# Performance work log

Measured on AMD Instinct MI355X. Metric: run time of the kernel, lower is better.

Reference implementation:

```python
import jax, jax.numpy as jnp
import numpy as np

B, H, W, C = 16, 64, 64, 256
C8 = C // 8

def setup_inputs() -> dict:
    key = jax.random.key(0)
    ks = jax.random.split(key, 8)
    return {
        "x": jax.random.normal(ks[0], (B, H, W, C), dtype=jnp.float32),
        "Wf": jax.random.normal(ks[1], (C, C8), dtype=jnp.float32) * 0.05,
        "Wg": jax.random.normal(ks[2], (C, C8), dtype=jnp.float32) * 0.05,
        "Wh": jax.random.normal(ks[3], (C, C), dtype=jnp.float32) * 0.05,
        "bf": jax.random.normal(ks[4], (C8,), dtype=jnp.float32) * 0.05,
        "bg": jax.random.normal(ks[5], (C8,), dtype=jnp.float32) * 0.05,
        "bh": jax.random.normal(ks[6], (C,), dtype=jnp.float32) * 0.05,
        "gamma": jax.random.normal(ks[7], (1,), dtype=jnp.float32) * 0.05,
    }

def reference(x, Wf, Wg, Wh, bf, bg, bh, gamma):
    # 1x1 convs == per-pixel channel matmuls (NHWC)
    f = jnp.einsum('bhwc,cd->bhwd', x, Wf) + bf  # [B,H,W,C/8]
    g = jnp.einsum('bhwc,cd->bhwd', x, Wg) + bg  # [B,H,W,C/8]
    h = jnp.einsum('bhwc,cd->bhwd', x, Wh) + bh  # [B,H,W,C]
    b = x.shape[0]
    # K.batch_flatten flattens all non-batch dims -> attention over BATCH dim
    gf = g.reshape(b, -1)                      # [B, HWC/8]
    ff = f.reshape(b, -1)                      # [B, HWC/8]
    hf = h.reshape(b, -1)                      # [B, HWC]
    s = gf @ ff.T                              # [B, B]
    beta = jax.nn.softmax(s, axis=-1)          # softmax over batch axis
    o = (beta @ hf).reshape(x.shape)           # [B,H,W,C]
    # activation=None -> linear; gamma-scaled residual
    return gamma * o + x
```

## Files before the change

### kernel.cpp

```cpp
#include <hip/hip_runtime.h>

typedef __attribute__((ext_vector_type(4))) float  f4;
typedef __attribute__((ext_vector_type(2))) float  f2;
typedef __attribute__((ext_vector_type(8))) short  short8;
typedef __attribute__((ext_vector_type(4))) float  f32x4;
typedef __attribute__((ext_vector_type(2))) unsigned int u32x2;

static __device__ __forceinline__ unsigned short f2bf(float f) {
    unsigned u = __builtin_bit_cast(unsigned, f);
    unsigned r = (u + 0x7FFFu + ((u >> 16) & 1u)) >> 16;
    return (unsigned short)r;
}
static __device__ __forceinline__ float bf2f(unsigned short h) {
    return __builtin_bit_cast(float, ((unsigned)h) << 16);
}

__global__ __launch_bounds__(256) void k_setup(const float* __restrict__ Wh,
                                               const float* __restrict__ bh,
                                               const float* __restrict__ Wf,
                                               const float* __restrict__ Wg,
                                               const float* __restrict__ gamma,
                                               unsigned short* __restrict__ WhT,
                                               float* __restrict__ gb,
                                               unsigned short* __restrict__ Wfg_hi,
                                               unsigned short* __restrict__ Wfg_lo) {
    __shared__ float T[8 * 260];
    const int t = threadIdx.x, b = blockIdx.x;
    const float g = gamma[0];
    if (b < 32) {
        const int c0 = b * 8;
        const int cr = t >> 5, q = t & 31;
        f4 v0 = *(const f4*)(Wh + (c0 + cr) * 256 + q * 8);
        f4 v1 = *(const f4*)(Wh + (c0 + cr) * 256 + q * 8 + 4);
        *(f4*)(T + cr * 260 + q * 8)     = v0;
        *(f4*)(T + cr * 260 + q * 8 + 4) = v1;
        __syncthreads();
        short8 o;
        #pragma unroll
        for (int j = 0; j < 8; ++j) o[j] = (short)f2bf(g * T[j * 260 + t]);
        *(short8*)(WhT + t * 256 + c0) = o;
    } else {
        gb[t] = g * bh[t];
        const int n = t >> 2, cq = t & 3;
        const float* Wsrc = (n < 32) ? Wf : Wg;
        const int nn = n & 31;
        #pragma unroll
        for (int c8 = 0; c8 < 8; ++c8) {
            short8 h8, l8;
            #pragma unroll
            for (int k = 0; k < 8; ++k) {
                const int c = cq * 64 + c8 * 8 + k;
                const float v = Wsrc[c * 32 + nn];
                const unsigned short h = f2bf(v);
                h8[k] = (short)h;
                l8[k] = (short)f2bf(v - bf2f(h));
            }
            *(short8*)(Wfg_hi + n * 256 + cq * 64 + c8 * 8) = h8;
            *(short8*)(Wfg_lo + n * 256 + cq * 64 + c8 * 8) = l8;
        }
    }
}

__global__ __launch_bounds__(256, 2) void ka(const float* __restrict__ x,
                                             const unsigned short* __restrict__ Wfg_hi,
                                             const unsigned short* __restrict__ Wfg_lo,
                                             const unsigned short* __restrict__ WhT,
                                             const float* __restrict__ bfv,
                                             const float* __restrict__ bgv,
                                             float* __restrict__ s_part,
                                             unsigned short* __restrict__ Hb) {
    __shared__ __align__(16) unsigned char smem[65536];

    const int t = threadIdx.x, w = t >> 6, l = t & 63;
    const int p = blockIdx.x * 4 + w;

    f4 xr[16];
    #pragma unroll
    for (int j = 0; j < 16; ++j)
        xr[j] = *(const f4*)(x + (((j << 12) + p) << 8) + l * 4);
    #pragma unroll
    for (int j = 0; j < 16; ++j) {
        const int r = j * 4 + w;
        int bo = r * 512 + l * 8;
        bo ^= (r & 7) << 4;
        const unsigned short h0 = f2bf(xr[j][0]), h1 = f2bf(xr[j][1]);
        const unsigned short h2 = f2bf(xr[j][2]), h3 = f2bf(xr[j][3]);
        u32x2 ph, pl;
        ph[0] = ((unsigned)h1 << 16) | h0;
        ph[1] = ((unsigned)h3 << 16) | h2;
        const unsigned short e0 = f2bf(xr[j][0] - bf2f(h0));
        const unsigned short e1 = f2bf(xr[j][1] - bf2f(h1));
        const unsigned short e2 = f2bf(xr[j][2] - bf2f(h2));
        const unsigned short e3 = f2bf(xr[j][3] - bf2f(h3));
        pl[0] = ((unsigned)e1 << 16) | e0;
        pl[1] = ((unsigned)e3 << 16) | e2;
        *(u32x2*)(smem + bo)         = ph;
        *(u32x2*)(smem + 32768 + bo) = pl;
    }
    __syncthreads();

    const int lrow = l & 15;
    const int hi4 = l >> 4;
    const int kfe  = hi4 * 8;
    const int ncol = w * 16 + lrow;
    f32x4 acc[4];
    f32x4 hacc[4][4];
    #pragma unroll
    for (int mt = 0; mt < 4; ++mt) {
        acc[mt] = (f32x4){0.f, 0.f, 0.f, 0.f};
        #pragma unroll
        for (int nt = 0; nt < 4; ++nt) hacc[mt][nt] = (f32x4){0.f, 0.f, 0.f, 0.f};
    }

    #pragma unroll
    for (int k0 = 0; k0 < 256; k0 += 32) {
        const short8 bh_ = *(const short8*)(Wfg_hi + ncol * 256 + k0 + kfe);
        const short8 bl_ = *(const short8*)(Wfg_lo + ncol * 256 + k0 + kfe);
        short8 ah[4], al[4];
        #pragma unroll
        for (int mt = 0; mt < 4; ++mt) {
            const int row = mt * 16 + lrow;
            int bo = row * 512 + (k0 + kfe) * 2;
            bo ^= (row & 7) << 4;
            ah[mt] = *(const short8*)(smem + bo);
            al[mt] = *(const short8*)(smem + 32768 + bo);
        }
        #pragma unroll
        for (int mt = 0; mt < 4; ++mt) {
            acc[mt] = __builtin_amdgcn_mfma_f32_16x16x32_bf16(ah[mt], bh_, acc[mt], 0, 0, 0);
            acc[mt] = __builtin_amdgcn_mfma_f32_16x16x32_bf16(al[mt], bh_, acc[mt], 0, 0, 0);
            acc[mt] = __builtin_amdgcn_mfma_f32_16x16x32_bf16(ah[mt], bl_, acc[mt], 0, 0, 0);
        }
        if (Hb) {
            short8 hb_[4];
            #pragma unroll
            for (int nt = 0; nt < 4; ++nt)
                hb_[nt] = *(const short8*)(WhT + (w * 64 + nt * 16 + lrow) * 256 + k0 + kfe);
            #pragma unroll
            for (int mt = 0; mt < 4; ++mt)
                #pragma unroll
                for (int nt = 0; nt < 4; ++nt)
                    hacc[mt][nt] = __builtin_amdgcn_mfma_f32_16x16x32_bf16(
                        ah[mt], hb_[nt], hacc[mt][nt], 0, 0, 0);
        }
    }

    if (Hb) {
        __syncthreads();
        #pragma unroll
        for (int mt = 0; mt < 4; ++mt) {
            const int j = mt * 4 + hi4;
            #pragma unroll
            for (int nt = 0; nt < 4; ++nt) {
                const int d = w * 64 + nt * 16 + lrow;
                #pragma unroll
                for (int jj = 0; jj < 4; ++jj)
                    *(unsigned short*)(smem + (jj * 16 + j) * 544 + d * 2) =
                        f2bf(hacc[mt][nt][jj]);
            }
        }
        __syncthreads();
        {
            const int r = t >> 2, q = t & 3;
            const int px = r >> 4, j = r & 15;
            unsigned short* dst = Hb + ((size_t)j * 4096 + blockIdx.x * 4 + px) * 256;
            #pragma unroll
            for (int cc = 0; cc < 8; ++cc) {
                const int chunk = (q * 8 + cc + r) & 31;
                f4 v = *(const f4*)(smem + r * 544 + chunk * 16);
                *(f4*)(dst + chunk * 8) = v;
            }
        }
    }
    __syncthreads();

    float* FG = (float*)smem;
    const float bias = (ncol < 32) ? bfv[ncol] : bgv[ncol - 32];
    #pragma unroll
    for (int mt = 0; mt < 4; ++mt)
        #pragma unroll
        for (int jj = 0; jj < 4; ++jj) {
            const int row = mt * 16 + hi4 * 4 + jj;
            FG[row * 68 + ncol] = acc[mt][jj] + bias;
        }
    __syncthreads();

    const int si = t >> 4, sj = t & 15;
    float sacc = 0.f;
    #pragma unroll
    for (int q = 0; q < 4; ++q) {
        const float* Gp = FG + (si * 4 + q) * 68 + 32;
        const float* Fp = FG + (sj * 4 + q) * 68;
        #pragma unroll
        for (int d4 = 0; d4 < 8; ++d4) {
            f4 gv = *(const f4*)(Gp + d4 * 4);
            f4 fv = *(const f4*)(Fp + d4 * 4);
            sacc += gv[0] * fv[0] + gv[1] * fv[1] + gv[2] * fv[2] + gv[3] * fv[3];
        }
    }
    s_part[blockIdx.x * 256 + si * 16 + sj] = sacc;
}

__global__ __launch_bounds__(256) void kb1(const float* __restrict__ s_part,
                                           float* __restrict__ s_red) {
    const int t = threadIdx.x, b = blockIdx.x;
    float a = 0.f;
    #pragma unroll
    for (int k = 0; k < 16; ++k) a += s_part[(b * 16 + k) * 256 + t];
    s_red[b * 256 + t] = a;
}

__global__ __launch_bounds__(1024) void kb2(const float* __restrict__ s_red,
                                            float* __restrict__ beta) {
    __shared__ float red[4 * 256];
    __shared__ float srow[256];
    __shared__ float erow[256];
    const int t = threadIdx.x;
    const int pair = t & 255;
    const int qr = t >> 8;
    float a = 0.f;
    #pragma unroll
    for (int b = qr * 16; b < qr * 16 + 16; ++b) a += s_red[b * 256 + pair];
    red[qr * 256 + pair] = a;
    __syncthreads();
    float s = 0.f, e = 0.f;
    if (t < 256) {
        s = red[pair] + red[256 + pair] + red[512 + pair] + red[768 + pair];
        srow[pair] = s;
    }
    __syncthreads();
    if (t < 256) {
        const int i = pair >> 4;
        float m = srow[i * 16];
        #pragma unroll
        for (int j = 1; j < 16; ++j) m = fmaxf(m, srow[i * 16 + j]);
        e = expf(s - m);
        erow[pair] = e;
    }
    __syncthreads();
    if (t < 256) {
        const int i = pair >> 4;
        float sum = 0.f;
        #pragma unroll
        for (int j = 0; j < 16; ++j) sum += erow[i * 16 + j];
        beta[pair] = e / sum;
    }
}

__global__ __launch_bounds__(256, 2) void kc(const float* __restrict__ x,
                                             const unsigned short* __restrict__ Hb,
                                             const float* __restrict__ gb,
                                             const float* __restrict__ beta,
                                             float* __restrict__ out) {
    __shared__ float beta_l[256];
    const int t = threadIdx.x, w = t >> 6, l = t & 63;
    const int p = blockIdx.x * 4 + w;
    const int cb = l * 4;

    if (t < 64) *(f4*)(beta_l + t * 4) = *(const f4*)(beta + t * 4);
    const f4 gb4 = *(const f4*)(gb + cb);

    u32x2 hb[16];
    #pragma unroll
    for (int j = 0; j < 16; ++j)
        hb[j] = *(const u32x2*)(Hb + ((size_t)j * 4096 + p) * 256 + cb);

    f4 acc[16];
    #pragma unroll
    for (int i = 0; i < 16; ++i)
        acc[i] = *(const f4*)(x + (((i << 12) + p) << 8) + cb) + gb4;
    __syncthreads();

    #pragma unroll
    for (int j4 = 0; j4 < 4; ++j4) {
        f4 h[4];
        #pragma unroll
        for (int jj = 0; jj < 4; ++jj) {
            const int j = j4 * 4 + jj;
            h[jj][0] = bf2f((unsigned short)(hb[j][0] & 0xffffu));
            h[jj][1] = bf2f((unsigned short)(hb[j][0] >> 16));
            h[jj][2] = bf2f((unsigned short)(hb[j][1] & 0xffffu));
            h[jj][3] = bf2f((unsigned short)(hb[j][1] >> 16));
        }
        #pragma unroll
        for (int i = 0; i < 16; ++i) {
            const f4 bv = *(const f4*)(beta_l + i * 16 + j4 * 4);
            acc[i] += h[0] * bv[0] + h[1] * bv[1] + h[2] * bv[2] + h[3] * bv[3];
        }
    }

    #pragma unroll
    for (int i = 0; i < 16; ++i) {
        const int idx = (((i << 12) + p) << 8) + cb;
        __builtin_nontemporal_store(acc[i], (f4*)(out + idx));
    }
}

__device__ __forceinline__ void kc_mix(const f4 (&xr)[16], const float* beta_l,
                                       unsigned char* stage, int w, int l) {
    #pragma unroll
    for (int i = 0; i < 16; ++i) {
        f4 bv0 = *(const f4*)(beta_l + i * 16);
        f4 bv1 = *(const f4*)(beta_l + i * 16 + 4);
        f4 bv2 = *(const f4*)(beta_l + i * 16 + 8);
        f4 bv3 = *(const f4*)(beta_l + i * 16 + 12);
        f4 a = {0.f, 0.f, 0.f, 0.f};
        #pragma unroll
        for (int j = 0; j < 4; ++j) {
            a += xr[j]      * bv0[j];
            a += xr[4 + j]  * bv1[j];
            a += xr[8 + j]  * bv2[j];
            a += xr[12 + j] * bv3[j];
        }
        const int r = i * 4 + w;
        int bo = r * 512 + l * 8;
        bo ^= (r & 7) << 4;
        u32x2 packed;
        packed[0] = ((unsigned)f2bf(a[1]) << 16) | f2bf(a[0]);
        packed[1] = ((unsigned)f2bf(a[3]) << 16) | f2bf(a[2]);
        *(u32x2*)(stage + bo) = packed;
    }
}

__device__ __forceinline__ void kc_gemm(f32x4 (&acc)[4][4], const unsigned char* stage,
                                        const unsigned short* wbase, int lrow, int kf) {
    #pragma unroll
    for (int mt = 0; mt < 4; ++mt)
        #pragma unroll
        for (int nt = 0; nt < 4; ++nt) acc[mt][nt] = (f32x4){0.f, 0.f, 0.f, 0.f};

    short8 bcur[4], bnxt[4];
    #pragma unroll
    for (int nt = 0; nt < 4; ++nt)
        bcur[nt] = *(const short8*)(wbase + nt * 16 * 256);

    #pragma unroll
    for (int ks = 0; ks < 8; ++ks) {
        const int k0 = ks * 32;
        if (ks < 7) {
            #pragma unroll
            for (int nt = 0; nt < 4; ++nt)
                bnxt[nt] = *(const short8*)(wbase + nt * 16 * 256 + k0 + 32);
        }
        short8 af[4];
        #pragma unroll
        for (int mt = 0; mt < 4; ++mt) {
            const int row = mt * 16 + lrow;
            int bo = row * 512 + (k0 + kf) * 2;
            bo ^= (row & 7) << 4;
            af[mt] = *(const short8*)(stage + bo);
        }
        #pragma unroll
        for (int mt = 0; mt < 4; ++mt)
            #pragma unroll
            for (int nt = 0; nt < 4; ++nt)
                acc[mt][nt] = __builtin_amdgcn_mfma_f32_16x16x32_bf16(
                    af[mt], bcur[nt], acc[mt][nt], 0, 0, 0);
        #pragma unroll
        for (int nt = 0; nt < 4; ++nt) bcur[nt] = bnxt[nt];
    }
}

__global__ __launch_bounds__(256, 3) void kc_fused(const float* __restrict__ x,
                                                   const unsigned short* __restrict__ WhT,
                                                   const float* __restrict__ gb,
                                                   const float* __restrict__ beta,
                                                   float* __restrict__ out) {
    __shared__ __align__(16) unsigned char smem[34048];
    float* beta_l = (float*)(smem + 33024);

    const int t = threadIdx.x;
    const int w = t >> 6;
    const int l = t & 63;
    const int p0 = blockIdx.x * 4;
    const int p  = p0 + w;
    const int cbase = l * 4;
    const int n0 = w * 64;
    const int lrow = l & 15;
    const int hi = l >> 4;
    const int kf = hi * 8;
    const unsigned short* wbase = WhT + (n0 + lrow) * 256 + kf;

    f4 xr[16];
    #pragma unroll
    for (int j = 0; j < 16; ++j)
        xr[j] = *(const f4*)(x + (((j << 12) + p) << 8) + cbase);
    if (t < 64) *(f4*)(beta_l + t * 4) = *(const f4*)(beta + t * 4);
    __syncthreads();

    kc_mix(xr, beta_l, smem, w, l);
    __syncthreads();

    f32x4 acc[4][4];
    kc_gemm(acc, smem, wbase, lrow, kf);

    float* cst = (float*)smem;
    const f4 gb4 = *(const f4*)(gb + cbase);
    #pragma unroll
    for (int h = 0; h < 2; ++h) {
        __syncthreads();
        #pragma unroll
        for (int mt2 = 0; mt2 < 2; ++mt2) {
            const int mt = h * 2 + mt2;
            #pragma unroll
            for (int nt = 0; nt < 4; ++nt)
                #pragma unroll
                for (int j = 0; j < 4; ++j) {
                    const int rl = mt2 * 16 + hi * 4 + j;
                    cst[rl * 258 + n0 + nt * 16 + lrow] = acc[mt][nt][j];
                }
        }
        __syncthreads();
        #pragma unroll
        for (int rr = 0; rr < 8; ++rr) {
            const int rl = rr * 4 + w;
            const int rg = h * 32 + rl;
            const int i  = rg >> 2, q = rg & 3;
            const int idx = (((i << 12) + p0 + q) << 8) + cbase;
            f4 o = *(const f4*)(cst + rl * 258 + cbase);
            o += gb4 + *(const f4*)(x + idx);
            __builtin_nontemporal_store(o, (f4*)(out + idx));
        }
    }
}

extern "C" void kernel_launch(void* const* d_in, const int* in_sizes, int n_in,
                              void* d_out, int out_size, void* d_ws, size_t ws_size,
                              hipStream_t stream) {
    const float* x     = (const float*)d_in[0];
    const float* Wf    = (const float*)d_in[1];
    const float* Wg    = (const float*)d_in[2];
    const float* Wh    = (const float*)d_in[3];
    const float* bfv   = (const float*)d_in[4];
    const float* bgv   = (const float*)d_in[5];
    const float* bhv   = (const float*)d_in[6];
    const float* gamma = (const float*)d_in[7];
    float* out = (float*)d_out;

    char* ws = (char*)d_ws;
    unsigned short* WhT = (unsigned short*)ws;
    float* gb     = (float*)(ws + 131072);
    float* beta   = (float*)(ws + 132096);
    float* s_part = (float*)(ws + 133120);
    unsigned short* Wfg_hi = (unsigned short*)(ws + 1181696);
    unsigned short* Wfg_lo = (unsigned short*)(ws + 1214464);
    float* s_red  = (float*)(ws + 1181696);
    unsigned short* Hbuf = (unsigned short*)(ws + 2097152);

    const bool big_ws = (ws_size >= 2097152ull + 33554432ull);
    unsigned short* HbArg = big_ws ? Hbuf : nullptr;

    k_setup<<<dim3(33), dim3(256), 0, stream>>>(Wh, bhv, Wf, Wg, gamma, WhT, gb, Wfg_hi, Wfg_lo);
    ka<<<dim3(1024), dim3(256), 0, stream>>>(x, Wfg_hi, Wfg_lo, WhT, bfv, bgv, s_part, HbArg);
    kb1<<<dim3(64), dim3(256), 0, stream>>>(s_part, s_red);
    kb2<<<dim3(1), dim3(1024), 0, stream>>>(s_red, beta);

    if (big_ws) {
        kc<<<dim3(1024), dim3(256), 0, stream>>>(x, Hbuf, gb, beta, out);
    } else {
        kc_fused<<<dim3(1024), dim3(256), 0, stream>>>(x, WhT, gb, beta, out);
    }
}
```

Before: 99.49 us.

## Split H projection into separate prefetched loop and merge epilogue barriers

Runs the f/g projection MFMA loop on its own, then runs the h projection in a second k-loop that prefetches the next WhT fragments from global memory while the current ones are used. hacc is no longer live during the f/g loop, which lowers register pressure. The FG score staging and the bf16 H staging now sit in disjoint LDS regions (FG at offset 0, H at offset 24576), so two __syncthreads are removed. The cost is that the x hi fragments are read from LDS a second time.

```diff
diff --git a/kernel.cpp b/kernel.cpp
--- a/kernel.cpp
+++ b/kernel.cpp
@@ -74,28 +74,30 @@
     const int t = threadIdx.x, w = t >> 6, l = t & 63;
     const int p = blockIdx.x * 4 + w;
 
-    f4 xr[16];
-    #pragma unroll
-    for (int j = 0; j < 16; ++j)
-        xr[j] = *(const f4*)(x + (((j << 12) + p) << 8) + l * 4);
-    #pragma unroll
-    for (int j = 0; j < 16; ++j) {
-        const int r = j * 4 + w;
-        int bo = r * 512 + l * 8;
-        bo ^= (r & 7) << 4;
-        const unsigned short h0 = f2bf(xr[j][0]), h1 = f2bf(xr[j][1]);
-        const unsigned short h2 = f2bf(xr[j][2]), h3 = f2bf(xr[j][3]);
-        u32x2 ph, pl;
-        ph[0] = ((unsigned)h1 << 16) | h0;
-        ph[1] = ((unsigned)h3 << 16) | h2;
-        const unsigned short e0 = f2bf(xr[j][0] - bf2f(h0));
-        const unsigned short e1 = f2bf(xr[j][1] - bf2f(h1));
-        const unsigned short e2 = f2bf(xr[j][2] - bf2f(h2));
-        const unsigned short e3 = f2bf(xr[j][3] - bf2f(h3));
-        pl[0] = ((unsigned)e1 << 16) | e0;
-        pl[1] = ((unsigned)e3 << 16) | e2;
-        *(u32x2*)(smem + bo)         = ph;
-        *(u32x2*)(smem + 32768 + bo) = pl;
+    {
+        f4 xr[16];
+        #pragma unroll
+        for (int j = 0; j < 16; ++j)
+            xr[j] = *(const f4*)(x + (((j << 12) + p) << 8) + l * 4);
+        #pragma unroll
+        for (int j = 0; j < 16; ++j) {
+            const int r = j * 4 + w;
+            int bo = r * 512 + l * 8;
+            bo ^= (r & 7) << 4;
+            const unsigned short h0 = f2bf(xr[j][0]), h1 = f2bf(xr[j][1]);
+            const unsigned short h2 = f2bf(xr[j][2]), h3 = f2bf(xr[j][3]);
+            u32x2 ph, pl;
+            ph[0] = ((unsigned)h1 << 16) | h0;
+            ph[1] = ((unsigned)h3 << 16) | h2;
+            const unsigned short e0 = f2bf(xr[j][0] - bf2f(h0));
+            const unsigned short e1 = f2bf(xr[j][1] - bf2f(h1));
+            const unsigned short e2 = f2bf(xr[j][2] - bf2f(h2));
+            const unsigned short e3 = f2bf(xr[j][3] - bf2f(h3));
+            pl[0] = ((unsigned)e1 << 16) | e0;
+            pl[1] = ((unsigned)e3 << 16) | e2;
+            *(u32x2*)(smem + bo)         = ph;
+            *(u32x2*)(smem + 32768 + bo) = pl;
+        }
     }
     __syncthreads();
 
@@ -103,14 +105,10 @@
     const int hi4 = l >> 4;
     const int kfe  = hi4 * 8;
     const int ncol = w * 16 + lrow;
+
     f32x4 acc[4];
-    f32x4 hacc[4][4];
-    #pragma unroll
-    for (int mt = 0; mt < 4; ++mt) {
-        acc[mt] = (f32x4){0.f, 0.f, 0.f, 0.f};
-        #pragma unroll
-        for (int nt = 0; nt < 4; ++nt) hacc[mt][nt] = (f32x4){0.f, 0.f, 0.f, 0.f};
-    }
+    #pragma unroll
+    for (int mt = 0; mt < 4; ++mt) acc[mt] = (f32x4){0.f, 0.f, 0.f, 0.f};
 
     #pragma unroll
     for (int k0 = 0; k0 < 256; k0 += 32) {
@@ -131,22 +129,60 @@
             acc[mt] = __builtin_amdgcn_mfma_f32_16x16x32_bf16(al[mt], bh_, acc[mt], 0, 0, 0);
             acc[mt] = __builtin_amdgcn_mfma_f32_16x16x32_bf16(ah[mt], bl_, acc[mt], 0, 0, 0);
         }
-        if (Hb) {
-            short8 hb_[4];
-            #pragma unroll
-            for (int nt = 0; nt < 4; ++nt)
-                hb_[nt] = *(const short8*)(WhT + (w * 64 + nt * 16 + lrow) * 256 + k0 + kfe);
+    }
+
+    f32x4 hacc[4][4];
+    if (Hb) {
+        #pragma unroll
+        for (int mt = 0; mt < 4; ++mt)
+            #pragma unroll
+            for (int nt = 0; nt < 4; ++nt) hacc[mt][nt] = (f32x4){0.f, 0.f, 0.f, 0.f};
+
+        const unsigned short* wbase = WhT + (w * 64 + lrow) * 256 + kfe;
+        short8 bcur[4], bnxt[4];
+        #pragma unroll
+        for (int nt = 0; nt < 4; ++nt)
+            bcur[nt] = *(const short8*)(wbase + nt * 16 * 256);
+
+        #pragma unroll
+        for (int ks = 0; ks < 8; ++ks) {
+            const int k0 = ks * 32;
+            if (ks < 7) {
+                #pragma unroll
+                for (int nt = 0; nt < 4; ++nt)
+                    bnxt[nt] = *(const short8*)(wbase + nt * 16 * 256 + k0 + 32);
+            }
+            short8 ah[4];
+            #pragma unroll
+            for (int mt = 0; mt < 4; ++mt) {
+                const int row = mt * 16 + lrow;
+                int bo = row * 512 + (k0 + kfe) * 2;
+                bo ^= (row & 7) << 4;
+                ah[mt] = *(const short8*)(smem + bo);
+            }
             #pragma unroll
             for (int mt = 0; mt < 4; ++mt)
                 #pragma unroll
                 for (int nt = 0; nt < 4; ++nt)
                     hacc[mt][nt] = __builtin_amdgcn_mfma_f32_16x16x32_bf16(
-                        ah[mt], hb_[nt], hacc[mt][nt], 0, 0, 0);
-        }
-    }
-
+                        ah[mt], bcur[nt], hacc[mt][nt], 0, 0, 0);
+            #pragma unroll
+            for (int nt = 0; nt < 4; ++nt) bcur[nt] = bnxt[nt];
+        }
+    }
+    __syncthreads();
+
+    float* FG = (float*)smem;
+    const float bias = (ncol < 32) ? bfv[ncol] : bgv[ncol - 32];
+    #pragma unroll
+    for (int mt = 0; mt < 4; ++mt)
+        #pragma unroll
+        for (int jj = 0; jj < 4; ++jj) {
+            const int row = mt * 16 + hi4 * 4 + jj;
+            FG[row * 68 + ncol] = acc[mt][jj] + bias;
+        }
     if (Hb) {
-        __syncthreads();
+        unsigned char* hst = smem + 24576;
         #pragma unroll
         for (int mt = 0; mt < 4; ++mt) {
             const int j = mt * 4 + hi4;
@@ -155,50 +191,41 @@
                 const int d = w * 64 + nt * 16 + lrow;
                 #pragma unroll
                 for (int jj = 0; jj < 4; ++jj)
-                    *(unsigned short*)(smem + (jj * 16 + j) * 544 + d * 2) =
+                    *(unsigned short*)(hst + (jj * 16 + j) * 544 + d * 2) =
                         f2bf(hacc[mt][nt][jj]);
             }
         }
-        __syncthreads();
-        {
-            const int r = t >> 2, q = t & 3;
-            const int px = r >> 4, j = r & 15;
-            unsigned short* dst = Hb + ((size_t)j * 4096 + blockIdx.x * 4 + px) * 256;
-            #pragma unroll
-            for (int cc = 0; cc < 8; ++cc) {
-                const int chunk = (q * 8 + cc + r) & 31;
-                f4 v = *(const f4*)(smem + r * 544 + chunk * 16);
-                *(f4*)(dst + chunk * 8) = v;
+    }
+    __syncthreads();
+
+    if (Hb) {
+        const int r = t >> 2, q = t & 3;
+        const int px = r >> 4, j = r & 15;
+        const unsigned char* hst = smem + 24576;
+        unsigned short* dst = Hb + ((size_t)j * 4096 + blockIdx.x * 4 + px) * 256;
+        #pragma unroll
+        for (int cc = 0; cc < 8; ++cc) {
+            const int chunk = (q * 8 + cc + r) & 31;
+            f4 v = *(const f4*)(hst + r * 544 + chunk * 16);
+            *(f4*)(dst + chunk * 8) = v;
+        }
+    }
+    {
+        const int si = t >> 4, sj = t & 15;
+        float sacc = 0.f;
+        #pragma unroll
+        for (int q = 0; q < 4; ++q) {
+            const float* Gp = FG + (si * 4 + q) * 68 + 32;
+            const float* Fp = FG + (sj * 4 + q) * 68;
+            #pragma unroll
+            for (int d4 = 0; d4 < 8; ++d4) {
+                f4 gv = *(const f4*)(Gp + d4 * 4);
+                f4 fv = *(const f4*)(Fp + d4 * 4);
+                sacc += gv[0] * fv[0] + gv[1] * fv[1] + gv[2] * fv[2] + gv[3] * fv[3];
             }
         }
-    }
-    __syncthreads();
-
-    float* FG = (float*)smem;
-    const float bias = (ncol < 32) ? bfv[ncol] : bgv[ncol - 32];
-    #pragma unroll
-    for (int mt = 0; mt < 4; ++mt)
-        #pragma unroll
-        for (int jj = 0; jj < 4; ++jj) {
-            const int row = mt * 16 + hi4 * 4 + jj;
-            FG[row * 68 + ncol] = acc[mt][jj] + bias;
-        }
-    __syncthreads();
-
-    const int si = t >> 4, sj = t & 15;
-    float sacc = 0.f;
-    #pragma unroll
-    for (int q = 0; q < 4; ++q) {
-        const float* Gp = FG + (si * 4 + q) * 68 + 32;
-        const float* Fp = FG + (sj * 4 + q) * 68;
-        #pragma unroll
-        for (int d4 = 0; d4 < 8; ++d4) {
-            f4 gv = *(const f4*)(Gp + d4 * 4);
-            f4 fv = *(const f4*)(Fp + d4 * 4);
-            sacc += gv[0] * fv[0] + gv[1] * fv[1] + gv[2] * fv[2] + gv[3] * fv[3];
-        }
-    }
-    s_part[blockIdx.x * 256 + si * 16 + sj] = sacc;
+        s_part[blockIdx.x * 256 + si * 16 + sj] = sacc;
+    }
 }
 
 __global__ __launch_bounds__(256) void kb1(const float* __restrict__ s_part,
```

Result: faster. 95.94 us (-3.6%).
